# Optimization experiments

Measured on AMD Instinct MI355X. Metric: run time of the kernel, lower is better.

Reference implementation:

```python
import jax, jax.numpy as jnp
import numpy as np

H = 1024   # hidden_size
V = 50257  # output_size (vocab)
B = 64     # batch
S = 256    # encoder seq len
NE = 7     # num_emotions


def setup_inputs() -> dict:
    key = jax.random.key(0)
    ks = jax.random.split(key, 16)
    def nrm(k, shape, scale=0.02):
        return jax.random.normal(k, shape, dtype=jnp.float32) * scale
    return {
        "input_step": jax.random.randint(ks[0], (1, B), 0, V),
        "input_step_emotion": jax.random.randint(ks[1], (1, B), 0, NE),
        "last_hidden": jax.random.normal(ks[2], (1, B, H), dtype=jnp.float32),
        "input_context": jax.random.normal(ks[3], (B, H), dtype=jnp.float32),
        "encoder_outputs": jax.random.normal(ks[4], (S, B, H), dtype=jnp.float32),
        "ememory": jax.random.randint(ks[5], (V,), 0, 2).astype(jnp.int32),
        "embedding": nrm(ks[6], (V, H)),
        "emotion_embedding": nrm(ks[7], (NE, H)),
        "W_read": nrm(ks[8], (H, 3 * H)), "b_read": jnp.zeros((H,), jnp.float32),
        "W_write": nrm(ks[9], (H, H)), "b_write": jnp.zeros((H,), jnp.float32),
        "W_ih": nrm(ks[10], (3 * H, 4 * H)), "W_hh": nrm(ks[11], (3 * H, H)),
        "b_ih": jnp.zeros((3 * H,), jnp.float32), "b_hh": jnp.zeros((3 * H,), jnp.float32),
        "W_concat": nrm(ks[12], (H, 2 * H)), "b_concat": jnp.zeros((H,), jnp.float32),
        "W_out": nrm(ks[13], (V, H)), "b_out": jnp.zeros((V,), jnp.float32),
        "W_alpha": nrm(ks[14], (1, V)), "b_alpha": jnp.zeros((1,), jnp.float32),
    }


def reference(input_step, input_step_emotion, last_hidden, input_context,
              encoder_outputs, ememory, embedding, emotion_embedding,
              W_read, b_read, W_write, b_write, W_ih, W_hh, b_ih, b_hh,
              W_concat, b_concat, W_out, b_out, W_alpha, b_alpha):
    Hd = last_hidden.shape[-1]
    # ---- ECM internal memory (read gate) ----
    emo = emotion_embedding[input_step_emotion]            # [1,B,H]
    lw = embedding[input_step]                             # [1,B,H]
    h_sum = jnp.sum(last_hidden, axis=0, keepdims=True)    # [1,B,H]
    ctx_in = input_context[None]                           # [1,B,H]
    M_read = jax.nn.sigmoid(jnp.concatenate([lw, h_sum, ctx_in], -1) @ W_read.T + b_read)
    emo_g = emo * M_read                                   # gated emotion state
    # ---- single GRU step (PyTorch gate order r,z,n) ----
    X = jnp.concatenate([lw, h_sum, ctx_in, emo_g], -1)[0]  # [B,4H]
    h0 = last_hidden[0]                                     # [B,H]
    gi = X @ W_ih.T + b_ih
    gh = h0 @ W_hh.T + b_hh
    r = jax.nn.sigmoid(gi[:, :Hd] + gh[:, :Hd])
    z = jax.nn.sigmoid(gi[:, Hd:2 * Hd] + gh[:, Hd:2 * Hd])
    n = jnp.tanh(gi[:, 2 * Hd:] + r * gh[:, 2 * Hd:])
    h_new = (1.0 - z) * n + z * h0                          # [B,H]
    rnn_output = h_new[None]                                # [1,B,H]
    hidden = h_new[None]
    # ---- write gate ----
    M_write = jax.nn.sigmoid(rnn_output @ W_write.T + b_write)
    new_M_emo = emo_g * M_write                             # [1,B,H]
    # ---- Luong dot attention ----
    scores = jnp.sum(rnn_output * encoder_outputs, axis=2).T  # [B,S]
    attn_w = jax.nn.softmax(scores, axis=1)
    context = jnp.einsum('bs,sbh->bh', attn_w, encoder_outputs)  # [B,H]
    concat_out = jnp.tanh(jnp.concatenate([h_new, context], 1) @ W_concat.T + b_concat)
    # ---- external memory gated dual softmax ----
    logits = concat_out @ W_out.T + b_out                   # [B,V]
    g = jax.nn.sigmoid(logits @ W_alpha.T + b_alpha)        # [B,1]
    mask = (ememory == 1)[None]                             # [1,V]
    NEG = jnp.float32(-1e9)
    # Equivalent to torch's mask-gather -> softmax -> scatter-back-by-sorted-idx:
    # softmax within each group, reassembled in original vocab order.
    se = jax.nn.softmax(jnp.where(mask, logits, NEG), axis=1)
    sg = jax.nn.softmax(jnp.where(mask, NEG, logits), axis=1)
    output = jnp.where(mask, se * g, sg * (1.0 - g))        # [B,V]
    return (output, hidden, new_M_emo, context)
```

## Files before the change

kernel.cpp:

```cpp
#include <hip/hip_runtime.h>
#include <hip/hip_bf16.h>
#include <math.h>

#define B 64
#define H 1024
#define SEQ 256
#define V 50257
#define NBLK 393

typedef float4 f4;
typedef __attribute__((ext_vector_type(4))) float f32x4;
typedef __attribute__((ext_vector_type(8))) short bf16x8;

__device__ inline float sigm(float x){ return 1.0f/(1.0f+expf(-x)); }
__device__ inline short f2bf(float x){
  __hip_bfloat16 h = __float2bfloat16(x);
  union { __hip_bfloat16 h; short s; } u; u.h = h; return u.s;
}
__device__ inline short2 cvt2(float x, float y){
  __hip_bfloat162 h = __float22bfloat162_rn(float2{x, y});
  union { __hip_bfloat162 h; short2 s; } u; u.h = h; return u.s;
}
__device__ inline bf16x8 pack8(f4 lo, f4 hi){
  union { bf16x8 v; short2 s[4]; } u;
  u.s[0]=cvt2(lo.x,lo.y); u.s[1]=cvt2(lo.z,lo.w);
  u.s[2]=cvt2(hi.x,hi.y); u.s[3]=cvt2(hi.z,hi.w);
  return u.v;
}
__device__ inline float wrsum(float v){
  #pragma unroll
  for(int o=32;o;o>>=1) v += __shfl_xor(v,o);
  return v;
}
__device__ inline float wrmax(float v){
  #pragma unroll
  for(int o=32;o;o>>=1) v = fmaxf(v,__shfl_xor(v,o));
  return v;
}
__device__ inline f32x4 mfma16(bf16x8 a, bf16x8 b, f32x4 c){
  return __builtin_amdgcn_mfma_f32_16x16x32_bf16(a,b,c,0,0,0);
}
__device__ inline void gll16(const void* g, void* l){
  __builtin_amdgcn_global_load_lds((const __attribute__((address_space(1))) void*)g,
                                   (__attribute__((address_space(3))) void*)l, 16, 0, 0);
}

__global__ void k_build(const int* __restrict__ istep,
                        const float* __restrict__ lasth, const float* __restrict__ ictx,
                        const float* __restrict__ emb, short* __restrict__ X_b){
  int b = blockIdx.x; int h = threadIdx.x*4;
  int iw = istep[b];
  f4 lw = *(const f4*)(emb  + (size_t)iw*H + h);
  f4 hs = *(const f4*)(lasth + (size_t)b*H + h);
  f4 cv = *(const f4*)(ictx + (size_t)b*H + h);
  short* xb = X_b + (size_t)b*4096;
  *(short4*)(xb +        h) = make_short4(f2bf(lw.x),f2bf(lw.y),f2bf(lw.z),f2bf(lw.w));
  *(short4*)(xb + 1024 + h) = make_short4(f2bf(hs.x),f2bf(hs.y),f2bf(hs.z),f2bf(hs.w));
  *(short4*)(xb + 2048 + h) = make_short4(f2bf(cv.x),f2bf(cv.y),f2bf(cv.z),f2bf(cv.w));
}

__launch_bounds__(256)
__global__ void k_pre(const int* __restrict__ iemo, const short* __restrict__ X_b,
                      const float* __restrict__ eemb,
                      const float* __restrict__ Wread, const float* __restrict__ bread,
                      const float* __restrict__ Whh,
                      float* __restrict__ emog, short* __restrict__ X_b_w,
                      float* __restrict__ gh){
  __shared__ float red[4][64][20];
  int tid = threadIdx.x;
  int w = tid>>6, l = tid&63, lm = l&15, lq = l>>4;
  f32x4 acc0={0,0,0,0}, acc1={0,0,0,0}, acc2={0,0,0,0}, acc3={0,0,0,0};
  int readmode = (blockIdx.x < 64);
  int tile = readmode ? blockIdx.x : (blockIdx.x - 64);
  int ncol = tile*16 + lm;
  const float* wp = readmode ? (Wread + (size_t)ncol*3072 + lq*8)
                             : (Whh   + (size_t)ncol*1024 + lq*8);
  const short* ap = readmode ? (X_b + lm*4096 + lq*8)
                             : (X_b + 1024 + lm*4096 + lq*8);
  int kbeg = readmode ? w*768 : w*256;
  int kend = readmode ? (kbeg + 768) : (kbeg + 256);
  for(int k0=kbeg; k0<kend; k0+=64){
    f4 w0 = *(const f4*)(wp + k0);
    f4 w1 = *(const f4*)(wp + k0 + 4);
    f4 w2 = *(const f4*)(wp + k0 + 32);
    f4 w3 = *(const f4*)(wp + k0 + 36);
    bf16x8 a00 = *(const bf16x8*)(ap + k0);
    bf16x8 a01 = *(const bf16x8*)(ap + k0 + 32);
    bf16x8 a10 = *(const bf16x8*)(ap + 16*4096 + k0);
    bf16x8 a11 = *(const bf16x8*)(ap + 16*4096 + k0 + 32);
    bf16x8 a20 = *(const bf16x8*)(ap + 32*4096 + k0);
    bf16x8 a21 = *(const bf16x8*)(ap + 32*4096 + k0 + 32);
    bf16x8 a30 = *(const bf16x8*)(ap + 48*4096 + k0);
    bf16x8 a31 = *(const bf16x8*)(ap + 48*4096 + k0 + 32);
    bf16x8 b0 = pack8(w0,w1), b1 = pack8(w2,w3);
    acc0 = mfma16(a00,b0,acc0); acc1 = mfma16(a10,b0,acc1);
    acc2 = mfma16(a20,b0,acc2); acc3 = mfma16(a30,b0,acc3);
    acc0 = mfma16(a01,b1,acc0); acc1 = mfma16(a11,b1,acc1);
    acc2 = mfma16(a21,b1,acc2); acc3 = mfma16(a31,b1,acc3);
  }
  #pragma unroll
  for(int r=0;r<4;r++){
    red[w][     lq*4+r][lm] = acc0[r];
    red[w][16 + lq*4+r][lm] = acc1[r];
    red[w][32 + lq*4+r][lm] = acc2[r];
    red[w][48 + lq*4+r][lm] = acc3[r];
  }
  __syncthreads();
  int m = tid>>2;
  if(readmode){
    int ie = iemo[m];
    #pragma unroll
    for(int j=0;j<4;j++){
      int c = (tid&3)*4 + j;
      float v = red[0][m][c]+red[1][m][c]+red[2][m][c]+red[3][m][c];
      int n = tile*16 + c;
      float s = sigm(v + bread[n]);
      float eg = s * eemb[(size_t)ie*1024 + n];
      emog[(size_t)m*1024 + n] = eg;
      X_b_w[(size_t)m*4096 + 3072 + n] = f2bf(eg);
    }
  } else {
    #pragma unroll
    for(int j=0;j<4;j++){
      int c = (tid&3)*4 + j;
      float v = red[0][m][c]+red[1][m][c]+red[2][m][c]+red[3][m][c];
      gh[(size_t)m*3072 + tile*16 + c] = v;
    }
  }
}

__launch_bounds__(256)
__global__ void k_gi(const short* __restrict__ X_b, const float* __restrict__ Wih,
                     float* __restrict__ gp){
  __shared__ float red[4][64][20];
  int tid = threadIdx.x;
  int w = tid>>6, l = tid&63, lm = l&15, lq = l>>4;
  int half = blockIdx.y;
  int ncol = blockIdx.x*16 + lm;
  const float* wp = Wih + (size_t)ncol*4096 + lq*8;
  const short* ap = X_b + lm*4096 + lq*8;
  int kbeg = half*2048 + w*512, kend = kbeg + 512;
  f32x4 acc0={0,0,0,0}, acc1={0,0,0,0}, acc2={0,0,0,0}, acc3={0,0,0,0};
  for(int k0=kbeg; k0<kend; k0+=64){
    f4 w0 = *(const f4*)(wp + k0);
    f4 w1 = *(const f4*)(wp + k0 + 4);
    f4 w2 = *(const f4*)(wp + k0 + 32);
    f4 w3 = *(const f4*)(wp + k0 + 36);
    bf16x8 a00 = *(const bf16x8*)(ap + k0);
    bf16x8 a01 = *(const bf16x8*)(ap + k0 + 32);
    bf16x8 a10 = *(const bf16x8*)(ap + 16*4096 + k0);
    bf16x8 a11 = *(const bf16x8*)(ap + 16*4096 + k0 + 32);
    bf16x8 a20 = *(const bf16x8*)(ap + 32*4096 + k0);
    bf16x8 a21 = *(const bf16x8*)(ap + 32*4096 + k0 + 32);
    bf16x8 a30 = *(const bf16x8*)(ap + 48*4096 + k0);
    bf16x8 a31 = *(const bf16x8*)(ap + 48*4096 + k0 + 32);
    bf16x8 b0 = pack8(w0,w1), b1 = pack8(w2,w3);
    acc0 = mfma16(a00,b0,acc0); acc1 = mfma16(a10,b0,acc1);
    acc2 = mfma16(a20,b0,acc2); acc3 = mfma16(a30,b0,acc3);
    acc0 = mfma16(a01,b1,acc0); acc1 = mfma16(a11,b1,acc1);
    acc2 = mfma16(a21,b1,acc2); acc3 = mfma16(a31,b1,acc3);
  }
  #pragma unroll
  for(int r=0;r<4;r++){
    red[w][     lq*4+r][lm] = acc0[r];
    red[w][16 + lq*4+r][lm] = acc1[r];
    red[w][32 + lq*4+r][lm] = acc2[r];
    red[w][48 + lq*4+r][lm] = acc3[r];
  }
  __syncthreads();
  int m = tid>>2;
  #pragma unroll
  for(int j=0;j<4;j++){
    int c = (tid&3)*4 + j;
    float v = red[0][m][c]+red[1][m][c]+red[2][m][c]+red[3][m][c];
    gp[(size_t)(half*64+m)*3072 + blockIdx.x*16 + c] = v;
  }
}

__global__ void k_gru(const float* __restrict__ gp, const float* __restrict__ gh,
                      const float* __restrict__ bih, const float* __restrict__ bhh,
                      const float* __restrict__ h0, float* __restrict__ hid,
                      short* __restrict__ hid_b, short* __restrict__ a2_b){
  int t = blockIdx.x*256 + threadIdx.x;
  int b = t>>8, j = (t&255)*4;
  const float* gi0 = gp + (size_t)b*3072 + j;
  const float* gi1 = gp + (size_t)(64+b)*3072 + j;
  const float* ghb = gh + (size_t)b*3072 + j;
  f4 h0v = *(const f4*)(h0 + (size_t)b*1024 + j);
  f4 hres; short4 hb;
  #pragma unroll
  for(int c=0;c<4;c++){
    float r = sigm(gi0[c]      + gi1[c]      + bih[j+c]      + ghb[c]      + bhh[j+c]);
    float z = sigm(gi0[1024+c] + gi1[1024+c] + bih[1024+j+c] + ghb[1024+c] + bhh[1024+j+c]);
    float n = tanhf(gi0[2048+c] + gi1[2048+c] + bih[2048+j+c] + r*(ghb[2048+c] + bhh[2048+j+c]));
    float hv = ((const float*)&h0v)[c];
    float h = (1.0f - z)*n + z*hv;
    ((float*)&hres)[c] = h;
    ((short*)&hb)[c] = f2bf(h);
  }
  *(f4*)(hid + (size_t)b*1024 + j) = hres;
  *(short4*)(hid_b + (size_t)b*1024 + j) = hb;
  *(short4*)(a2_b + (size_t)b*2048 + j) = hb;
}

__launch_bounds__(256)
__global__ void k_flash(const float* __restrict__ enc, const float* __restrict__ hid,
                        float* __restrict__ part, float* __restrict__ ml,
                        const short* __restrict__ hid_b,
                        const float* __restrict__ Wwrite, const float* __restrict__ bwrite,
                        const float* __restrict__ emog, float* __restrict__ memo){
  __shared__ float red[4][64][20];
  int tid = threadIdx.x;
  int w = tid>>6, l = tid&63;
  if(blockIdx.x < 512){
    int b = blockIdx.x>>3, c = blockIdx.x&7;
    int chunk = c*4 + w;
    const float* hp = hid + (size_t)b*1024 + l*16;
    f4 q0 = *(const f4*)(hp), q1 = *(const f4*)(hp+4);
    f4 q2 = *(const f4*)(hp+8), q3 = *(const f4*)(hp+12);
    f4 cx0={0,0,0,0}, cx1={0,0,0,0}, cx2={0,0,0,0}, cx3={0,0,0,0};
    float mx = -1e30f, ls = 0.0f;
    int s0 = c*32 + w*8;
    for(int si=0; si<8; si++){
      const float* ep = enc + ((size_t)(s0+si)*64 + b)*1024 + l*16;
      f4 e0 = *(const f4*)(ep),   e1 = *(const f4*)(ep+4);
      f4 e2 = *(const f4*)(ep+8), e3 = *(const f4*)(ep+12);
      float d = e0.x*q0.x + e0.y*q0.y + e0.z*q0.z + e0.w*q0.w
              + e1.x*q1.x + e1.y*q1.y + e1.z*q1.z + e1.w*q1.w
              + e2.x*q2.x + e2.y*q2.y + e2.z*q2.z + e2.w*q2.w
              + e3.x*q3.x + e3.y*q3.y + e3.z*q3.z + e3.w*q3.w;
      d = wrsum(d);
      float mn = fmaxf(mx, d);
      float a = expf(mx - mn), p = expf(d - mn);
      ls = ls*a + p;
      cx0.x = cx0.x*a + p*e0.x; cx0.y = cx0.y*a + p*e0.y;
      cx0.z = cx0.z*a + p*e0.z; cx0.w = cx0.w*a + p*e0.w;
      cx1.x = cx1.x*a + p*e1.x; cx1.y = cx1.y*a + p*e1.y;
      cx1.z = cx1.z*a + p*e1.z; cx1.w = cx1.w*a + p*e1.w;
      cx2.x = cx2.x*a + p*e2.x; cx2.y = cx2.y*a + p*e2.y;
      cx2.z = cx2.z*a + p*e2.z; cx2.w = cx2.w*a + p*e2.w;
      cx3.x = cx3.x*a + p*e3.x; cx3.y = cx3.y*a + p*e3.y;
      cx3.z = cx3.z*a + p*e3.z; cx3.w = cx3.w*a + p*e3.w;
      mx = mn;
    }
    float* pp = part + ((size_t)b*32 + chunk)*1024 + l*16;
    *(f4*)(pp)    = cx0; *(f4*)(pp+4)  = cx1;
    *(f4*)(pp+8)  = cx2; *(f4*)(pp+12) = cx3;
    if(l==0){ ml[((size_t)b*32+chunk)*2] = mx; ml[((size_t)b*32+chunk)*2+1] = ls; }
  } else {
    int tile = blockIdx.x - 512;
    int lm = l&15, lq = l>>4;
    int ncol = tile*16 + lm;
    const float* wp = Wwrite + (size_t)ncol*1024 + lq*8;
    const short* ap = hid_b + lm*1024 + lq*8;
    int kbeg = w*256, kend = kbeg + 256;
    f32x4 acc0={0,0,0,0}, acc1={0,0,0,0}, acc2={0,0,0,0}, acc3={0,0,0,0};
    for(int k0=kbeg; k0<kend; k0+=64){
      f4 w0 = *(const f4*)(wp + k0);
      f4 w1 = *(const f4*)(wp + k0 + 4);
      f4 w2 = *(const f4*)(wp + k0 + 32);
      f4 w3 = *(const f4*)(wp + k0 + 36);
      bf16x8 a00 = *(const bf16x8*)(ap + k0);
      bf16x8 a01 = *(const bf16x8*)(ap + k0 + 32);
      bf16x8 a10 = *(const bf16x8*)(ap + 16*1024 + k0);
      bf16x8 a11 = *(const bf16x8*)(ap + 16*1024 + k0 + 32);
      bf16x8 a20 = *(const bf16x8*)(ap + 32*1024 + k0);
      bf16x8 a21 = *(const bf16x8*)(ap + 32*1024 + k0 + 32);
      bf16x8 a30 = *(const bf16x8*)(ap + 48*1024 + k0);
      bf16x8 a31 = *(const bf16x8*)(ap + 48*1024 + k0 + 32);
      bf16x8 b0 = pack8(w0,w1), b1 = pack8(w2,w3);
      acc0 = mfma16(a00,b0,acc0); acc1 = mfma16(a10,b0,acc1);
      acc2 = mfma16(a20,b0,acc2); acc3 = mfma16(a30,b0,acc3);
      acc0 = mfma16(a01,b1,acc0); acc1 = mfma16(a11,b1,acc1);
      acc2 = mfma16(a21,b1,acc2); acc3 = mfma16(a31,b1,acc3);
    }
    #pragma unroll
    for(int r=0;r<4;r++){
      red[w][     lq*4+r][lm] = acc0[r];
      red[w][16 + lq*4+r][lm] = acc1[r];
      red[w][32 + lq*4+r][lm] = acc2[r];
      red[w][48 + lq*4+r][lm] = acc3[r];
    }
    __syncthreads();
    int m = tid>>2;
    #pragma unroll
    for(int j=0;j<4;j++){
      int c = (tid&3)*4 + j;
      float v = red[0][m][c]+red[1][m][c]+red[2][m][c]+red[3][m][c];
      int n = tile*16 + c;
      memo[(size_t)m*1024 + n] = sigm(v + bwrite[n]) * emog[(size_t)m*1024 + n];
    }
  }
}

__global__ void k_ctxr(const float* __restrict__ part, const float* __restrict__ ml,
                       float* __restrict__ ctxo, short* __restrict__ a2_b){
  int b = blockIdx.x; int t = threadIdx.x;
  __shared__ float sscale[32];
  if(t < 64){
    float mc = (t<32) ? ml[((size_t)b*32+t)*2]   : -1e30f;
    float lc = (t<32) ? ml[((size_t)b*32+t)*2+1] : 0.0f;
    float M = wrmax(mc);
    float L = wrsum(lc * expf(mc - M));
    if(t<32) sscale[t] = expf(mc - M) / L;
  }
  __syncthreads();
  int h = t*4;
  f4 acc = {0,0,0,0};
  for(int c=0;c<32;c++){
    f4 p = *(const f4*)(part + ((size_t)b*32 + c)*1024 + h);
    float s = sscale[c];
    acc.x += s*p.x; acc.y += s*p.y; acc.z += s*p.z; acc.w += s*p.w;
  }
  *(f4*)(ctxo + (size_t)b*1024 + h) = acc;
  *(short4*)(a2_b + (size_t)b*2048 + 1024 + h) =
      make_short4(f2bf(acc.x),f2bf(acc.y),f2bf(acc.z),f2bf(acc.w));
}

__launch_bounds__(256)
__global__ void k_cc(const short* __restrict__ a2_b, const float* __restrict__ Wc,
                     const float* __restrict__ bc, short* __restrict__ cc_b){
  __shared__ float red[4][64][20];
  int tid = threadIdx.x;
  int w = tid>>6, l = tid&63, lm = l&15, lq = l>>4;
  int ncol = blockIdx.x*16 + lm;
  const float* wp = Wc + (size_t)ncol*2048 + lq*8;
  const short* ap = a2_b + lm*2048 + lq*8;
  int kbeg = w*512, kend = kbeg + 512;
  f32x4 acc0={0,0,0,0}, acc1={0,0,0,0}, acc2={0,0,0,0}, acc3={0,0,0,0};
  for(int k0=kbeg; k0<kend; k0+=64){
    f4 w0 = *(const f4*)(wp + k0);
    f4 w1 = *(const f4*)(wp + k0 + 4);
    f4 w2 = *(const f4*)(wp + k0 + 32);
    f4 w3 = *(const f4*)(wp + k0 + 36);
    bf16x8 a00 = *(const bf16x8*)(ap + k0);
    bf16x8 a01 = *(const bf16x8*)(ap + k0 + 32);
    bf16x8 a10 = *(const bf16x8*)(ap + 16*2048 + k0);
    bf16x8 a11 = *(const bf16x8*)(ap + 16*2048 + k0 + 32);
    bf16x8 a20 = *(const bf16x8*)(ap + 32*2048 + k0);
    bf16x8 a21 = *(const bf16x8*)(ap + 32*2048 + k0 + 32);
    bf16x8 a30 = *(const bf16x8*)(ap + 48*2048 + k0);
    bf16x8 a31 = *(const bf16x8*)(ap + 48*2048 + k0 + 32);
    bf16x8 b0 = pack8(w0,w1), b1 = pack8(w2,w3);
    acc0 = mfma16(a00,b0,acc0); acc1 = mfma16(a10,b0,acc1);
    acc2 = mfma16(a20,b0,acc2); acc3 = mfma16(a30,b0,acc3);
    acc0 = mfma16(a01,b1,acc0); acc1 = mfma16(a11,b1,acc1);
    acc2 = mfma16(a21,b1,acc2); acc3 = mfma16(a31,b1,acc3);
  }
  #pragma unroll
  for(int r=0;r<4;r++){
    red[w][     lq*4+r][lm] = acc0[r];
    red[w][16 + lq*4+r][lm] = acc1[r];
    red[w][32 + lq*4+r][lm] = acc2[r];
    red[w][48 + lq*4+r][lm] = acc3[r];
  }
  __syncthreads();
  int m = tid>>2;
  #pragma unroll
  for(int j=0;j<4;j++){
    int c = (tid&3)*4 + j;
    float v = red[0][m][c]+red[1][m][c]+red[2][m][c]+red[3][m][c];
    int n = blockIdx.x*16 + c;
    cc_b[(size_t)m*1024 + n] = f2bf(tanhf(v + bc[n]));
  }
}

__launch_bounds__(256)
__global__ void k_out(const short* __restrict__ A, const float* __restrict__ Wm,
                      const float* __restrict__ bias, const float* __restrict__ wal,
                      const int* __restrict__ mem,
                      float* __restrict__ outf, float* __restrict__ pstat){
  __shared__ float Wt[2][128][64];
  __shared__ short At[2][64][64];
  float (*sst)[64][6] = (float (*)[64][6])(&At[0][0][0]);
  int tid = threadIdx.x;
  int w = tid>>6, l = tid&63;
  int lm = l&15, lq = l>>4;
  int n0 = blockIdx.x*128;

  int wRl = l>>4, wSeg = l&15;
  int aRl = l>>3, aSeg = l&7;

  f32x4 accA0={0,0,0,0}, accA1={0,0,0,0}, accA2={0,0,0,0}, accA3={0,0,0,0};
  f32x4 accB0={0,0,0,0}, accB1={0,0,0,0}, accB2={0,0,0,0}, accB3={0,0,0,0};

  {
    #pragma unroll
    for(int i=0;i<8;i++){
      int R = w*32 + i*4 + wRl;
      int gr = n0 + R; if(gr > V-1) gr = V-1;
      const float* gp = Wm + (size_t)gr*1024 + (size_t)(wSeg ^ (R&7))*4;
      gll16(gp, &Wt[0][w*32 + i*4][0]);
    }
    #pragma unroll
    for(int j=0;j<2;j++){
      int R = w*16 + j*8 + aRl;
      const short* gp = A + (size_t)R*1024 + (size_t)(aSeg ^ (R&7))*8;
      gll16(gp, &At[0][w*16 + j*8][0]);
    }
  }
  __syncthreads();

  int buf = 0;
  for(int step=0; step<16; step++){
    if(step < 15){
      int k0 = (step+1)*64;
      #pragma unroll
      for(int i=0;i<8;i++){
        int R = w*32 + i*4 + wRl;
        int gr = n0 + R; if(gr > V-1) gr = V-1;
        const float* gp = Wm + (size_t)gr*1024 + k0 + (size_t)(wSeg ^ (R&7))*4;
        gll16(gp, &Wt[buf^1][w*32 + i*4][0]);
      }
      #pragma unroll
      for(int j=0;j<2;j++){
        int R = w*16 + j*8 + aRl;
        const short* gp = A + (size_t)R*1024 + k0 + (size_t)(aSeg ^ (R&7))*8;
        gll16(gp, &At[buf^1][w*16 + j*8][0]);
      }
    }
    int wrow0 = w*32 + lm, wx0 = wrow0 & 7;
    int wrow1 = w*32 + 16 + lm, wx1 = wrow1 & 7;
    #pragma unroll
    for(int h=0; h<2; h++){
      f4 lo0 = *(const f4*)(&Wt[buf][wrow0][((h*8 + lq*2  ) ^ wx0)*4]);
      f4 hi0 = *(const f4*)(&Wt[buf][wrow0][((h*8 + lq*2+1) ^ wx0)*4]);
      bf16x8 bfr0 = pack8(lo0, hi0);
      f4 lo1 = *(const f4*)(&Wt[buf][wrow1][((h*8 + lq*2  ) ^ wx1)*4]);
      f4 hi1 = *(const f4*)(&Wt[buf][wrow1][((h*8 + lq*2+1) ^ wx1)*4]);
      bf16x8 bfr1 = pack8(lo1, hi1);
      #pragma unroll
      for(int rr=0; rr<4; rr++){
        int arow = rr*16 + lm;
        int as = (h*4 + lq) ^ (arow & 7);
        bf16x8 afr = *(const bf16x8*)(&At[buf][arow][as*8]);
        if(rr==0){ accA0 = mfma16(afr,bfr0,accA0); accB0 = mfma16(afr,bfr1,accB0); }
        else if(rr==1){ accA1 = mfma16(afr,bfr0,accA1); accB1 = mfma16(afr,bfr1,accB1); }
        else if(rr==2){ accA2 = mfma16(afr,bfr0,accA2); accB2 = mfma16(afr,bfr1,accB2); }
        else { accA3 = mfma16(afr,bfr0,accA3); accB3 = mfma16(afr,bfr1,accB3); }
      }
    }
    __syncthreads();
    buf ^= 1;
  }

  for(int cg2=0; cg2<2; cg2++){
    int ncol = n0 + w*32 + cg2*16 + lm;
    float bv=0.0f, wv=0.0f; int mv=-1;
    if(ncol < V){ bv = bias[ncol]; wv = wal[ncol]; mv = mem[ncol]; }
    #pragma unroll
    for(int qi=0; qi<4; qi++){
      #pragma unroll
      for(int r=0;r<4;r++){
        float v;
        if(cg2==0){
          if(qi==0) v = accA0[r]; else if(qi==1) v = accA1[r];
          else if(qi==2) v = accA2[r]; else v = accA3[r];
        } else {
          if(qi==0) v = accB0[r]; else if(qi==1) v = accB1[r];
          else if(qi==2) v = accB2[r]; else v = accB3[r];
        }
        v += bv;
        int row = lq*4 + r + 16*qi;
        if(ncol < V) outf[(size_t)row*V + ncol] = v;
        float dd = v*wv;
        float em = (mv==1) ? v : -1e30f;
        float gm = (mv==0) ? v : -1e30f;
        #pragma unroll
        for(int o=1;o<16;o<<=1){
          dd += __shfl_xor(dd,o);
          em = fmaxf(em, __shfl_xor(em,o));
          gm = fmaxf(gm, __shfl_xor(gm,o));
        }
        float pe = (mv==1) ? expf(v - em) : 0.0f;
        float pg = (mv==0) ? expf(v - gm) : 0.0f;
        #pragma unroll
        for(int o=1;o<16;o<<=1){
          pe += __shfl_xor(pe,o);
          pg += __shfl_xor(pg,o);
        }
        if(lm==0){
          sst[w*2+cg2][row][0]=dd; sst[w*2+cg2][row][1]=em; sst[w*2+cg2][row][2]=pe;
          sst[w*2+cg2][row][3]=gm; sst[w*2+cg2][row][4]=pg;
        }
      }
    }
  }
  __syncthreads();
  if(tid < 64){
    float dd=0.0f, me=-1e30f, se=0.0f, mg=-1e30f, sg=0.0f;
    #pragma unroll
    for(int g=0; g<8; g++){
      dd += sst[g][tid][0];
      float m2=sst[g][tid][1], s2=sst[g][tid][2];
      float nm=fmaxf(me,m2); se = se*expf(me-nm) + s2*expf(m2-nm); me = nm;
      m2=sst[g][tid][3]; s2=sst[g][tid][4];
      nm=fmaxf(mg,m2); sg = sg*expf(mg-nm) + s2*expf(m2-nm); mg = nm;
    }
    float* pp = pstat + ((size_t)tid*NBLK + blockIdx.x)*6;
    pp[0]=dd; pp[1]=me; pp[2]=se; pp[3]=mg; pp[4]=sg;
  }
}

__global__ void k_merge(const float* __restrict__ pstat, float* __restrict__ stats){
  int b = blockIdx.x, t = threadIdx.x;
  float dd=0.0f, me=-1e30f, se=0.0f, mg=-1e30f, sg=0.0f;
  for(int i=t; i<NBLK; i+=256){
    const float* pp = pstat + ((size_t)b*NBLK + i)*6;
    dd += pp[0];
    float m2=pp[1], s2=pp[2];
    float nm=fmaxf(me,m2); se = se*expf(me-nm) + s2*expf(m2-nm); me = nm;
    m2=pp[3]; s2=pp[4];
    nm=fmaxf(mg,m2); sg = sg*expf(mg-nm) + s2*expf(m2-nm); mg = nm;
  }
  #pragma unroll
  for(int o=32;o;o>>=1){
    dd += __shfl_xor(dd,o);
    float m2=__shfl_xor(me,o), s2=__shfl_xor(se,o);
    float nm=fmaxf(me,m2); se = se*expf(me-nm) + s2*expf(m2-nm); me = nm;
    m2=__shfl_xor(mg,o); s2=__shfl_xor(sg,o);
    nm=fmaxf(mg,m2); sg = sg*expf(mg-nm) + s2*expf(m2-nm); mg = nm;
  }
  __shared__ float sm[4][5];
  int wv = t>>6;
  if((t&63)==0){ sm[wv][0]=dd; sm[wv][1]=me; sm[wv][2]=se; sm[wv][3]=mg; sm[wv][4]=sg; }
  __syncthreads();
  if(t==0){
    float D=0, M=-1e30f, S=0, M2=-1e30f, S2=0;
    for(int i=0;i<4;i++){
      D += sm[i][0];
      float m = fmaxf(M, sm[i][1]); S  = S*expf(M-m)  + sm[i][2]*expf(sm[i][1]-m);  M = m;
      float n = fmaxf(M2,sm[i][3]); S2 = S2*expf(M2-n)+ sm[i][4]*expf(sm[i][3]-n); M2 = n;
    }
    stats[b*8+0]=D; stats[b*8+1]=M; stats[b*8+2]=M2; stats[b*8+3]=S; stats[b*8+4]=S2;
  }
}

__global__ void k_final(float* __restrict__ logits, const int* __restrict__ mem,
                        const float* __restrict__ stats, const float* __restrict__ balpha){
  int v = blockIdx.x*256 + threadIdx.x;
  int b = blockIdx.y;
  if(v >= V) return;
  float dot = stats[b*8+0], me = stats[b*8+1], mg = stats[b*8+2];
  float se = stats[b*8+3],  sg = stats[b*8+4];
  float g = sigm(dot + balpha[0]);
  float l = logits[(size_t)b*V + v];
  float o = (mem[v]==1) ? (expf(l-me)/se * g) : (expf(l-mg)/sg * (1.0f-g));
  logits[(size_t)b*V + v] = o;
}

extern "C" void kernel_launch(void* const* d_in, const int* in_sizes, int n_in,
                              void* d_out, int out_size, void* d_ws, size_t ws_size,
                              hipStream_t stream){
  const int*   istep   = (const int*)d_in[0];
  const int*   iemo    = (const int*)d_in[1];
  const float* lasth   = (const float*)d_in[2];
  const float* ictx    = (const float*)d_in[3];
  const float* enc     = (const float*)d_in[4];
  const int*   emem    = (const int*)d_in[5];
  const float* emb     = (const float*)d_in[6];
  const float* eemb    = (const float*)d_in[7];
  const float* W_read  = (const float*)d_in[8];
  const float* b_read  = (const float*)d_in[9];
  const float* W_write = (const float*)d_in[10];
  const float* b_write = (const float*)d_in[11];
  const float* W_ih    = (const float*)d_in[12];
  const float* W_hh    = (const float*)d_in[13];
  const float* b_ih    = (const float*)d_in[14];
  const float* b_hh    = (const float*)d_in[15];
  const float* W_concat= (const float*)d_in[16];
  const float* b_concat= (const float*)d_in[17];
  const float* W_out   = (const float*)d_in[18];
  const float* b_out   = (const float*)d_in[19];
  const float* W_alpha = (const float*)d_in[20];
  const float* b_alpha = (const float*)d_in[21];

  short* X_b  = (short*)d_ws;
  float* emog = (float*)((char*)d_ws + 524288);
  float* gp   = emog + 65536;
  float* gh   = gp + 393216;
  float* part = gh + 196608;
  float* ml   = part + 2097152;
  float* stats= ml + 4096;
  float* pstat= stats + 512;
  short* hid_b= (short*)(pstat + 64*NBLK*6);
  short* a2_b = hid_b + 65536;
  short* cc_b = a2_b + 131072;

  float* out0 = (float*)d_out;
  float* hid  = out0 + (size_t)B*V;
  float* memo = hid + 65536;
  float* ctxo = memo + 65536;

  k_build<<<64,256,0,stream>>>(istep, lasth, ictx, emb, X_b);
  k_pre  <<<256,256,0,stream>>>(iemo, X_b, eemb, W_read, b_read, W_hh, emog, X_b, gh);
  k_gi   <<<dim3(192,2),256,0,stream>>>(X_b, W_ih, gp);
  k_gru  <<<64,256,0,stream>>>(gp, gh, b_ih, b_hh, lasth, hid, hid_b, a2_b);
  k_flash<<<576,256,0,stream>>>(enc, hid, part, ml, hid_b, W_write, b_write, emog, memo);
  k_ctxr <<<64,256,0,stream>>>(part, ml, ctxo, a2_b);
  k_cc   <<<64,256,0,stream>>>(a2_b, W_concat, b_concat, cc_b);
  k_out  <<<NBLK,256,0,stream>>>(cc_b, W_out, b_out, W_alpha, emem, out0, pstat);
  k_merge<<<64,256,0,stream>>>(pstat, stats);
  k_final<<<dim3(197,64),256,0,stream>>>(out0, emem, stats, b_alpha);
}
```

Measured before the change: 184.3 us.

## Triple-stage W_out loads with vmcnt waits and fuse merge into final kernel

The output GEMM now keeps two K-slices in flight. It waits with explicit s_waitcnt vmcnt counts and raw barriers instead of __syncthreads, which drains all outstanding loads. Separately, the per-row stats merge is folded into k_final: every one of the 197x64 blocks recomputes the 393-entry reduction itself, which removes one kernel launch and the stats round trip. This adds redundant reduction work per block and relies on the hand-set vmcnt value matching the number of issued loads.

```diff
diff --git a/kernel.cpp b/kernel.cpp
--- a/kernel.cpp
+++ b/kernel.cpp
@@ -384,41 +384,32 @@
   f32x4 accA0={0,0,0,0}, accA1={0,0,0,0}, accA2={0,0,0,0}, accA3={0,0,0,0};
   f32x4 accB0={0,0,0,0}, accB1={0,0,0,0}, accB2={0,0,0,0}, accB3={0,0,0,0};
 
-  {
+  auto stage = [&](int k0, int bsel){
     #pragma unroll
     for(int i=0;i<8;i++){
       int R = w*32 + i*4 + wRl;
       int gr = n0 + R; if(gr > V-1) gr = V-1;
-      const float* gp = Wm + (size_t)gr*1024 + (size_t)(wSeg ^ (R&7))*4;
-      gll16(gp, &Wt[0][w*32 + i*4][0]);
+      const float* gp = Wm + (size_t)gr*1024 + k0 + (size_t)(wSeg ^ (R&7))*4;
+      gll16(gp, &Wt[bsel][w*32 + i*4][0]);
     }
     #pragma unroll
     for(int j=0;j<2;j++){
       int R = w*16 + j*8 + aRl;
-      const short* gp = A + (size_t)R*1024 + (size_t)(aSeg ^ (R&7))*8;
-      gll16(gp, &At[0][w*16 + j*8][0]);
-    }
-  }
-  __syncthreads();
-
-  int buf = 0;
+      const short* gp = A + (size_t)R*1024 + k0 + (size_t)(aSeg ^ (R&7))*8;
+      gll16(gp, &At[bsel][w*16 + j*8][0]);
+    }
+  };
+
+  stage(0, 0);
+  stage(64, 1);
+
   for(int step=0; step<16; step++){
-    if(step < 15){
-      int k0 = (step+1)*64;
-      #pragma unroll
-      for(int i=0;i<8;i++){
-        int R = w*32 + i*4 + wRl;
-        int gr = n0 + R; if(gr > V-1) gr = V-1;
-        const float* gp = Wm + (size_t)gr*1024 + k0 + (size_t)(wSeg ^ (R&7))*4;
-        gll16(gp, &Wt[buf^1][w*32 + i*4][0]);
-      }
-      #pragma unroll
-      for(int j=0;j<2;j++){
-        int R = w*16 + j*8 + aRl;
-        const short* gp = A + (size_t)R*1024 + k0 + (size_t)(aSeg ^ (R&7))*8;
-        gll16(gp, &At[buf^1][w*16 + j*8][0]);
-      }
-    }
+    if(step < 15) asm volatile("s_waitcnt vmcnt(10)" ::: "memory");
+    else          asm volatile("s_waitcnt vmcnt(0)"  ::: "memory");
+    __builtin_amdgcn_s_barrier();
+    asm volatile("" ::: "memory");
+
+    int buf = step & 1;
     int wrow0 = w*32 + lm, wx0 = wrow0 & 7;
     int wrow1 = w*32 + 16 + lm, wx1 = wrow1 & 7;
     #pragma unroll
@@ -440,8 +431,10 @@
         else { accA3 = mfma16(afr,bfr0,accA3); accB3 = mfma16(afr,bfr1,accB3); }
       }
     }
-    __syncthreads();
-    buf ^= 1;
+
+    asm volatile("" ::: "memory");
+    __builtin_amdgcn_s_barrier();
+    if(step < 14) stage((step+2)*64, buf);
   }
 
   for(int cg2=0; cg2<2; cg2++){
@@ -502,8 +495,10 @@
   }
 }
 
-__global__ void k_merge(const float* __restrict__ pstat, float* __restrict__ stats){
-  int b = blockIdx.x, t = threadIdx.x;
+__global__ void k_final(float* __restrict__ logits, const int* __restrict__ mem,
+                        const float* __restrict__ pstat, const float* __restrict__ balpha){
+  int b = blockIdx.y;
+  int t = threadIdx.x;
   float dd=0.0f, me=-1e30f, se=0.0f, mg=-1e30f, sg=0.0f;
   for(int i=t; i<NBLK; i+=256){
     const float* pp = pstat + ((size_t)b*NBLK + i)*6;
@@ -522,6 +517,7 @@
     nm=fmaxf(mg,m2); sg = sg*expf(mg-nm) + s2*expf(m2-nm); mg = nm;
   }
   __shared__ float sm[4][5];
+  __shared__ float fin[5];
   int wv = t>>6;
   if((t&63)==0){ sm[wv][0]=dd; sm[wv][1]=me; sm[wv][2]=se; sm[wv][3]=mg; sm[wv][4]=sg; }
   __syncthreads();
@@ -532,21 +528,17 @@
       float m = fmaxf(M, sm[i][1]); S  = S*expf(M-m)  + sm[i][2]*expf(sm[i][1]-m);  M = m;
       float n = fmaxf(M2,sm[i][3]); S2 = S2*expf(M2-n)+ sm[i][4]*expf(sm[i][3]-n); M2 = n;
     }
-    stats[b*8+0]=D; stats[b*8+1]=M; stats[b*8+2]=M2; stats[b*8+3]=S; stats[b*8+4]=S2;
-  }
-}
-
-__global__ void k_final(float* __restrict__ logits, const int* __restrict__ mem,
-                        const float* __restrict__ stats, const float* __restrict__ balpha){
-  int v = blockIdx.x*256 + threadIdx.x;
-  int b = blockIdx.y;
-  if(v >= V) return;
-  float dot = stats[b*8+0], me = stats[b*8+1], mg = stats[b*8+2];
-  float se = stats[b*8+3],  sg = stats[b*8+4];
+    fin[0]=D; fin[1]=M; fin[2]=M2; fin[3]=S; fin[4]=S2;
+  }
+  __syncthreads();
+  float dot = fin[0], meF = fin[1], mgF = fin[2], seF = fin[3], sgF = fin[4];
   float g = sigm(dot + balpha[0]);
-  float l = logits[(size_t)b*V + v];
-  float o = (mem[v]==1) ? (expf(l-me)/se * g) : (expf(l-mg)/sg * (1.0f-g));
-  logits[(size_t)b*V + v] = o;
+  int v = blockIdx.x*256 + t;
+  if(v < V){
+    float lg = logits[(size_t)b*V + v];
+    float o = (mem[v]==1) ? (expf(lg-meF)/seF * g) : (expf(lg-mgF)/sgF * (1.0f-g));
+    logits[(size_t)b*V + v] = o;
+  }
 }
 
 extern "C" void kernel_launch(void* const* d_in, const int* in_sizes, int n_in,
@@ -581,8 +573,7 @@
   float* gh   = gp + 393216;
   float* part = gh + 196608;
   float* ml   = part + 2097152;
-  float* stats= ml + 4096;
-  float* pstat= stats + 512;
+  float* pstat= ml + 4096;
   short* hid_b= (short*)(pstat + 64*NBLK*6);
   short* a2_b = hid_b + 65536;
   short* cc_b = a2_b + 131072;
@@ -600,6 +591,5 @@
   k_ctxr <<<64,256,0,stream>>>(part, ml, ctxo, a2_b);
   k_cc   <<<64,256,0,stream>>>(a2_b, W_concat, b_concat, cc_b);
   k_out  <<<NBLK,256,0,stream>>>(cc_b, W_out, b_out, W_alpha, emem, out0, pstat);
-  k_merge<<<64,256,0,stream>>>(pstat, stats);
-  k_final<<<dim3(197,64),256,0,stream>>>(out0, emem, stats, b_alpha);
-}
+  k_final<<<dim3(197,64),256,0,stream>>>(out0, emem, pstat, b_alpha);
+}
```

After: 214.0 us. 1.16x slower.
